# Optimization experiments

Hardware: AMD Instinct MI355X
Metric: run time of the kernel (lower is better)

The kernel has to match this reference:

```python
import jax, jax.numpy as jnp
from jax import lax
import numpy as np

K = 3          # kernel size
KK = K * K
PAD = 1
STRIDE = 1
DIL = 1


def _bilinear_gather(img, ys, xs):
    # img: [B,C,H,W]; ys/xs: [B,KK,Ho,Wo] float sample coords.
    # torchvision deform_conv2d bilinear: zero outside, corner-wise validity.
    B, C, H, W = img.shape
    y0f = jnp.floor(ys)
    x0f = jnp.floor(xs)
    ly = ys - y0f
    lx = xs - x0f
    y0 = y0f.astype(jnp.int32)
    x0 = x0f.astype(jnp.int32)

    def corner(yi, xi):
        valid = (yi >= 0) & (yi < H) & (xi >= 0) & (xi < W)
        yc = jnp.clip(yi, 0, H - 1)
        xc = jnp.clip(xi, 0, W - 1)
        g = jax.vmap(lambda im, y, x: im[:, y, x])(img, yc, xc)  # [B,C,KK,Ho,Wo]
        return g * valid[:, None].astype(img.dtype)

    w00 = ((1 - ly) * (1 - lx))[:, None]
    w01 = ((1 - ly) * lx)[:, None]
    w10 = (ly * (1 - lx))[:, None]
    w11 = (ly * lx)[:, None]
    out = corner(y0, x0) * w00
    out = out + corner(y0, x0 + 1) * w01
    out = out + corner(y0 + 1, x0) * w10
    out = out + corner(y0 + 1, x0 + 1) * w11
    return out  # [B,C,KK,Ho,Wo]


def _deform_conv_forward(x, weight, bias, pg_w, pg_b):
    B, C, H, W = x.shape
    O = weight.shape[0]
    # offset/mask generator: 3x3 conv, stride 1, pad 1 -> [B, 3*KK, H, W]
    params = lax.conv_general_dilated(
        x, pg_w, window_strides=(1, 1), padding=[(1, 1), (1, 1)],
        dimension_numbers=('NCHW', 'OIHW', 'NCHW'))
    params = params + pg_b[None, :, None, None]
    oh, ow, m = jnp.split(params, 3, axis=1)          # each [B,KK,H,W]
    offset = jnp.concatenate([oh, ow], axis=1)        # [B,2*KK,H,W] (as in module)
    mask = jax.nn.sigmoid(m)                          # [B,KK,H,W]

    Ho = (H + 2 * PAD - DIL * (K - 1) - 1) // STRIDE + 1
    Wo = (W + 2 * PAD - DIL * (K - 1) - 1) // STRIDE + 1

    # torchvision layout: channel 2n = dy, 2n+1 = dx for kernel slot n
    off = offset.reshape(B, KK, 2, Ho, Wo)
    dy = off[:, :, 0]  # [B,KK,Ho,Wo]
    dx = off[:, :, 1]

    n = jnp.arange(KK)
    ki = (n // K).astype(x.dtype)   # kernel row offset
    kj = (n % K).astype(x.dtype)    # kernel col offset
    oy = (jnp.arange(Ho, dtype=x.dtype) * STRIDE - PAD)
    ox = (jnp.arange(Wo, dtype=x.dtype) * STRIDE - PAD)
    ys = oy[None, None, :, None] + (DIL * ki)[None, :, None, None] + dy
    xs = ox[None, None, None, :] + (DIL * kj)[None, :, None, None] + dx

    sampled = _bilinear_gather(x, ys, xs)             # [B,C,KK,Ho,Wo]
    sampled = sampled * mask[:, None]                 # modulated (DCNv2)

    w = weight.reshape(O, C, KK)
    out = jnp.einsum('bckhw,ock->bohw', sampled, w)
    out = out + bias[None, :, None, None]
    return out


def setup_inputs() -> dict:
    key = jax.random.key(0)
    k1, k2, k3, k4 = jax.random.split(key, 4)
    B, C, H, W, O = 4, 64, 128, 128, 64
    x = jax.random.normal(k1, (B, C, H, W), dtype=jnp.float32)
    weight = jax.random.normal(k2, (O, C, K, K), dtype=jnp.float32) * 0.05
    bias = jax.random.normal(k3, (O,), dtype=jnp.float32) * 0.05
    pg_w = jax.random.normal(k4, (3 * KK, C, 3, 3), dtype=jnp.float32) * 0.01
    pg_b = jnp.zeros((3 * KK,), dtype=jnp.float32)
    return {'x': x, 'weight': weight, 'bias': bias, 'pg_w': pg_w, 'pg_b': pg_b}


def reference(x, weight, bias, pg_w, pg_b):
    return _deform_conv_forward(x, weight, bias, pg_w, pg_b)
```

## Files before the change

### kernel.cpp

```cpp
#include <hip/hip_runtime.h>
#include <hip/hip_fp16.h>
#include <math.h>


typedef __attribute__((ext_vector_type(8))) short short8;
typedef __attribute__((ext_vector_type(8))) _Float16 f16x8;
typedef __attribute__((ext_vector_type(4))) float f32x4;

#define PSTR 2088

__device__ __forceinline__ unsigned short f2h(float f) {
    union { __half h; unsigned short s; } v; v.h = __float2half_rn(f); return v.s;
}
__device__ __forceinline__ f16x8 s2f(short8 s) {
    union { short8 s; f16x8 f; } u; u.s = s; return u.f;
}
__device__ __forceinline__ __half2 u2h2(unsigned u) {
    union { unsigned u; __half2 h; } v; v.u = u; return v.h;
}
__device__ __forceinline__ unsigned h22u(__half2 h) {
    union { __half2 h; unsigned u; } v; v.h = h; return v.u;
}
__device__ __forceinline__ unsigned uget(const uint4& v, int p) {
    return p == 0 ? v.x : p == 1 ? v.y : p == 2 ? v.z : v.w;
}

__global__ __launch_bounds__(256) void k_prep(const float* __restrict__ x,
                                              unsigned short* __restrict__ xh,
                                              const float* __restrict__ weight,
                                              const float* __restrict__ pg_w,
                                              unsigned short* __restrict__ wtF,
                                              unsigned short* __restrict__ pgwF) {
    __shared__ float tile[64][33];
    int bid = blockIdx.x;
    int t = threadIdx.x;
    if (bid < 2048) {
        int b = bid >> 9, h = (bid >> 2) & 127, w0 = (bid & 3) * 32;
        for (int idx = t; idx < 2048; idx += 256) {
            int c = idx >> 5, w = idx & 31;
            tile[c][w] = x[((b * 64 + c) * 128 + h) * 128 + w0 + w];
        }
        __syncthreads();
        {
            int wl = t >> 3, c0 = (t & 7) * 8;
            short8 v;
#pragma unroll
            for (int e = 0; e < 8; ++e) v[e] = (short)f2h(tile[c0 + e][wl]);
            *(short8*)&xh[(((size_t)b * 128 + h) * 128 + w0 + wl) * 64 + c0] = v;
        }
    } else {
        int idx = (bid - 2048) * 256 + t;
        if (idx < 36864) {
            int e = idx & 7, l = (idx >> 3) & 63, grp = idx >> 9;
            int nt = grp & 3, kb = (grp >> 2) & 1, kk = grp >> 3;
            int ln = l & 15, quad = l >> 4;
            int o = nt * 16 + ln;
            int c = kb * 32 + quad * 8 + e;
            wtF[idx] = f2h(weight[(o * 64 + c) * 9 + kk]);
        }
        int i2 = idx - 36864;
        if (i2 >= 0 && i2 < 18432) {
            int e = i2 & 7, l = (i2 >> 3) & 63, grp = i2 >> 9;
            int tl = grp & 1, kb = grp >> 1;
            int ln = l & 15, quad = l >> 4;
            int p = tl * 16 + ln;
            int k = kb * 32 + quad * 8 + e;
            float v = 0.f;
            if (p < 27) {
                int q = k >> 6, c = k & 63;
                v = pg_w[(p * 64 + c) * 9 + q];
            }
            pgwF[i2] = f2h(v);
        }
    }
}

__global__ __launch_bounds__(512, 4) void k_fused(const unsigned short* __restrict__ xh,
                                                  const unsigned short* __restrict__ pgwF,
                                                  const float* __restrict__ pg_b,
                                                  const unsigned short* __restrict__ wtF,
                                                  const float* __restrict__ bias,
                                                  float* __restrict__ out) {
    __shared__ unsigned short patch[8 * PSTR];
    __shared__ float P_s[27 * 129];

    int bid = blockIdx.x;
    int b  = bid >> 7;
    int h0 = ((bid >> 3) & 15) * 8;
    int w0 = (bid & 7) * 16;
    int t = threadIdx.x;
    int base_y = h0 - 2, base_x = w0 - 2;
    const unsigned short* xbb = xh + (size_t)b * 16384 * 64;

    for (int i = t; i < 2080; i += 512) {
        int yy = i / 160;
        int r  = i - yy * 160;
        int xx = r >> 3;
        int cg = r & 7;
        int gy = base_y + yy, gx = base_x + xx;
        int pos = yy * 20 + xx;
        short8 v = (short8)0;
        if (((unsigned)gy < 128u) && ((unsigned)gx < 128u))
            v = *(const short8*)&xbb[(gy * 128 + gx) * 64 + cg * 8];
        *(short8*)&patch[cg * PSTR + pos * 8] = v;
    }
    __syncthreads();

    int l = t & 63, w = t >> 6;
    int quad = l >> 4, ln = l & 15;
    int px = w * 16 + ln;
    int hh = h0 + w, ww = w0 + ln;

    {
        f32x4 o0 = {0.f, 0.f, 0.f, 0.f}, o1 = {0.f, 0.f, 0.f, 0.f};
#pragma unroll
        for (int kb = 0; kb < 18; ++kb) {
            int q = kb >> 1;
            int kh = q / 3, kw = q - 3 * (q / 3);
            short8 b0 = *(const short8*)&pgwF[(kb * 2 + 0) * 512 + l * 8];
            short8 b1 = *(const short8*)&pgwF[(kb * 2 + 1) * 512 + l * 8];
            int aoff = (w + kh + 1) * 20 + (ln + kw + 1);
            int cg = (kb & 1) * 4 + quad;
            short8 af = *(const short8*)&patch[cg * PSTR + aoff * 8];
            o0 = __builtin_amdgcn_mfma_f32_16x16x32_f16(s2f(af), s2f(b0), o0, 0, 0, 0);
            o1 = __builtin_amdgcn_mfma_f32_16x16x32_f16(s2f(af), s2f(b1), o1, 0, 0, 0);
        }
#pragma unroll
        for (int tile = 0; tile < 2; ++tile) {
            int p = tile * 16 + ln;
            f32x4 a = tile ? o1 : o0;
            if (p < 27) {
                float bo = pg_b[p];
#pragma unroll
                for (int i = 0; i < 4; ++i) {
                    int wpx = w * 16 + quad * 4 + i;
                    float v = a[i] + bo;
                    if (p >= 18) v = 1.f / (1.f + expf(-v));
                    P_s[p * 129 + wpx] = v;
                }
            }
        }
    }
    __syncthreads();

    f32x4 acc[4];
#pragma unroll
    for (int nt = 0; nt < 4; ++nt) acc[nt] = (f32x4){0.f, 0.f, 0.f, 0.f};

    int qbase = quad * PSTR;

#pragma unroll
    for (int kk = 0; kk < 9; ++kk) {
        short8 bfr[2][4];
#pragma unroll
        for (int kb = 0; kb < 2; ++kb)
#pragma unroll
            for (int nt = 0; nt < 4; ++nt)
                bfr[kb][nt] = *(const short8*)&wtF[((kk * 2 + kb) * 4 + nt) * 512 + l * 8];

        int ki = kk / 3, kj = kk - 3 * (kk / 3);
        float dyv = P_s[(2 * kk) * 129 + px];
        float dxv = P_s[(2 * kk + 1) * 129 + px];
        float m   = P_s[(18 + kk) * 129 + px];
        float ys = (float)(hh - 1 + ki) + dyv;
        float xs = (float)(ww - 1 + kj) + dxv;
        float y0f = floorf(ys), x0f = floorf(xs);
        int y0 = (int)y0f, x0 = (int)x0f;
        float ly = ys - y0f, lx = xs - x0f;
        float v0y = ((unsigned)y0 < 128u) ? 1.f : 0.f;
        float v1y = ((unsigned)(y0 + 1) < 128u) ? 1.f : 0.f;
        float v0x = ((unsigned)x0 < 128u) ? 1.f : 0.f;
        float v1x = ((unsigned)(x0 + 1) < 128u) ? 1.f : 0.f;
        float w00 = (1.f - ly) * (1.f - lx) * v0y * v0x * m;
        float w01 = (1.f - ly) * lx * v0y * v1x * m;
        float w10 = ly * (1.f - lx) * v1y * v0x * m;
        float w11 = ly * lx * v1y * v1x * m;
        int ly0 = y0 - base_y, lx0 = x0 - base_x;
        bool inp = ((unsigned)ly0 < 12u) && ((unsigned)lx0 < 18u);

        uint4 r[2][4];
        if (inp) {
            int pb = qbase + (ly0 * 20 + lx0) * 8;
#pragma unroll
            for (int kb = 0; kb < 2; ++kb) {
                int base = pb + kb * 4 * PSTR;
                r[kb][0] = *(const uint4*)&patch[base];
                r[kb][1] = *(const uint4*)&patch[base + 8];
                r[kb][2] = *(const uint4*)&patch[base + 160];
                r[kb][3] = *(const uint4*)&patch[base + 168];
            }
        } else {
            int y0c = min(max(y0, 0), 127), y1c = min(max(y0 + 1, 0), 127);
            int x0c = min(max(x0, 0), 127), x1c = min(max(x0 + 1, 0), 127);
            int base00 = (y0c * 128 + x0c) * 64;
            int dxo = (x1c - x0c) * 64, dyo = (y1c - y0c) * 8192;
#pragma unroll
            for (int kb = 0; kb < 2; ++kb) {
                int c0 = kb * 32 + quad * 8;
                r[kb][0] = *(const uint4*)&xbb[base00 + c0];
                r[kb][1] = *(const uint4*)&xbb[base00 + dxo + c0];
                r[kb][2] = *(const uint4*)&xbb[base00 + dyo + c0];
                r[kb][3] = *(const uint4*)&xbb[base00 + dyo + dxo + c0];
            }
        }

        __half2 W00 = __float2half2_rn(w00), W01 = __float2half2_rn(w01);
        __half2 W10 = __float2half2_rn(w10), W11 = __float2half2_rn(w11);
        f16x8 af[2];
#pragma unroll
        for (int kb = 0; kb < 2; ++kb) {
            union { unsigned u[4]; f16x8 f; } afu;
#pragma unroll
            for (int p = 0; p < 4; ++p) {
                __half2 v = __hmul2(W00, u2h2(uget(r[kb][0], p)));
                v = __hfma2(W01, u2h2(uget(r[kb][1], p)), v);
                v = __hfma2(W10, u2h2(uget(r[kb][2], p)), v);
                v = __hfma2(W11, u2h2(uget(r[kb][3], p)), v);
                afu.u[p] = h22u(v);
            }
            af[kb] = afu.f;
        }

#pragma unroll
        for (int kb = 0; kb < 2; ++kb)
#pragma unroll
            for (int nt = 0; nt < 4; ++nt)
                acc[nt] = __builtin_amdgcn_mfma_f32_16x16x32_f16(af[kb], s2f(bfr[kb][nt]), acc[nt], 0, 0, 0);
    }

    int ehh = h0 + w, eww = w0 + quad * 4;
#pragma unroll
    for (int nt = 0; nt < 4; ++nt) {
        int o = nt * 16 + ln;
        float bo = bias[o];
        float4 v;
        v.x = acc[nt][0] + bo; v.y = acc[nt][1] + bo;
        v.z = acc[nt][2] + bo; v.w = acc[nt][3] + bo;
        *(float4*)&out[((size_t)b * 64 + o) * 16384 + ehh * 128 + eww] = v;
    }
}

extern "C" void kernel_launch(void* const* d_in, const int* in_sizes, int n_in,
                              void* d_out, int out_size, void* d_ws, size_t ws_size,
                              hipStream_t stream) {
    const float* x      = (const float*)d_in[0];
    const float* weight = (const float*)d_in[1];
    const float* bias   = (const float*)d_in[2];
    const float* pg_w   = (const float*)d_in[3];
    const float* pg_b   = (const float*)d_in[4];
    float* out = (float*)d_out;

    unsigned short* xhB  = (unsigned short*)d_ws;
    unsigned short* wtF  = xhB + (size_t)4 * 16384 * 64;
    unsigned short* pgwF = wtF + 36864;

    k_prep<<<2264, 256, 0, stream>>>(x, xhB, weight, pg_w, wtF, pgwF);
    k_fused<<<512, 512, 0, stream>>>(xhB, pgwF, pg_b, wtF, bias, out);
}
```

Before: 98.93 us.

## Drop NHWC fp16 pre-pass; load and convert fp32 NCHW input directly into LDS patch

Removes the separate transpose/convert pass that wrote an NHWC fp16 copy of x to workspace. The fused kernel now reads fp32 NCHW directly when filling its LDS patch, converting pairs of channels to fp16 in place. Out-of-patch bilinear samples gather 32 scalar fp32 loads per corner set instead of vector fp16 loads. It also drops the unroll on the kk loop and the occupancy hint in launch bounds. This saves a full-tensor round trip through global memory and a launch, but makes the patch fill and the fallback gathers uncoalesced and more load-heavy.

```diff
diff --git a/kernel.cpp b/kernel.cpp
--- a/kernel.cpp
+++ b/kernel.cpp
@@ -25,62 +25,41 @@
     return p == 0 ? v.x : p == 1 ? v.y : p == 2 ? v.z : v.w;
 }
 
-__global__ __launch_bounds__(256) void k_prep(const float* __restrict__ x,
-                                              unsigned short* __restrict__ xh,
-                                              const float* __restrict__ weight,
+__global__ __launch_bounds__(256) void k_pack(const float* __restrict__ weight,
                                               const float* __restrict__ pg_w,
                                               unsigned short* __restrict__ wtF,
                                               unsigned short* __restrict__ pgwF) {
-    __shared__ float tile[64][33];
-    int bid = blockIdx.x;
-    int t = threadIdx.x;
-    if (bid < 2048) {
-        int b = bid >> 9, h = (bid >> 2) & 127, w0 = (bid & 3) * 32;
-        for (int idx = t; idx < 2048; idx += 256) {
-            int c = idx >> 5, w = idx & 31;
-            tile[c][w] = x[((b * 64 + c) * 128 + h) * 128 + w0 + w];
-        }
-        __syncthreads();
-        {
-            int wl = t >> 3, c0 = (t & 7) * 8;
-            short8 v;
-#pragma unroll
-            for (int e = 0; e < 8; ++e) v[e] = (short)f2h(tile[c0 + e][wl]);
-            *(short8*)&xh[(((size_t)b * 128 + h) * 128 + w0 + wl) * 64 + c0] = v;
-        }
-    } else {
-        int idx = (bid - 2048) * 256 + t;
-        if (idx < 36864) {
-            int e = idx & 7, l = (idx >> 3) & 63, grp = idx >> 9;
-            int nt = grp & 3, kb = (grp >> 2) & 1, kk = grp >> 3;
-            int ln = l & 15, quad = l >> 4;
-            int o = nt * 16 + ln;
-            int c = kb * 32 + quad * 8 + e;
-            wtF[idx] = f2h(weight[(o * 64 + c) * 9 + kk]);
-        }
-        int i2 = idx - 36864;
-        if (i2 >= 0 && i2 < 18432) {
-            int e = i2 & 7, l = (i2 >> 3) & 63, grp = i2 >> 9;
-            int tl = grp & 1, kb = grp >> 1;
-            int ln = l & 15, quad = l >> 4;
-            int p = tl * 16 + ln;
-            int k = kb * 32 + quad * 8 + e;
-            float v = 0.f;
-            if (p < 27) {
-                int q = k >> 6, c = k & 63;
-                v = pg_w[(p * 64 + c) * 9 + q];
-            }
-            pgwF[i2] = f2h(v);
-        }
-    }
-}
-
-__global__ __launch_bounds__(512, 4) void k_fused(const unsigned short* __restrict__ xh,
-                                                  const unsigned short* __restrict__ pgwF,
-                                                  const float* __restrict__ pg_b,
-                                                  const unsigned short* __restrict__ wtF,
-                                                  const float* __restrict__ bias,
-                                                  float* __restrict__ out) {
+    int idx = blockIdx.x * 256 + threadIdx.x;
+    if (idx < 36864) {
+        int e = idx & 7, l = (idx >> 3) & 63, grp = idx >> 9;
+        int nt = grp & 3, kb = (grp >> 2) & 1, kk = grp >> 3;
+        int ln = l & 15, quad = l >> 4;
+        int o = nt * 16 + ln;
+        int c = kb * 32 + quad * 8 + e;
+        wtF[idx] = f2h(weight[(o * 64 + c) * 9 + kk]);
+    }
+    int i2 = idx - 36864;
+    if (i2 >= 0 && i2 < 18432) {
+        int e = i2 & 7, l = (i2 >> 3) & 63, grp = i2 >> 9;
+        int tl = grp & 1, kb = grp >> 1;
+        int ln = l & 15, quad = l >> 4;
+        int p = tl * 16 + ln;
+        int k = kb * 32 + quad * 8 + e;
+        float v = 0.f;
+        if (p < 27) {
+            int q = k >> 6, c = k & 63;
+            v = pg_w[(p * 64 + c) * 9 + q];
+        }
+        pgwF[i2] = f2h(v);
+    }
+}
+
+__global__ __launch_bounds__(512) void k_fused(const float* __restrict__ x,
+                                               const unsigned short* __restrict__ pgwF,
+                                               const float* __restrict__ pg_b,
+                                               const unsigned short* __restrict__ wtF,
+                                               const float* __restrict__ bias,
+                                               float* __restrict__ out) {
     __shared__ unsigned short patch[8 * PSTR];
     __shared__ float P_s[27 * 129];
 
@@ -90,19 +69,23 @@
     int w0 = (bid & 7) * 16;
     int t = threadIdx.x;
     int base_y = h0 - 2, base_x = w0 - 2;
-    const unsigned short* xbb = xh + (size_t)b * 16384 * 64;
-
-    for (int i = t; i < 2080; i += 512) {
-        int yy = i / 160;
-        int r  = i - yy * 160;
-        int xx = r >> 3;
-        int cg = r & 7;
+    const float* xb0 = x + (size_t)b * 64 * 16384;
+
+    for (int i = t; i < 8320; i += 512) {
+        int cp  = i / 260;
+        int rem = i - cp * 260;
+        int yy  = rem / 20;
+        int xx  = rem - yy * 20;
         int gy = base_y + yy, gx = base_x + xx;
+        unsigned u = 0;
+        if (((unsigned)gy < 128u) && ((unsigned)gx < 128u)) {
+            int c = cp * 2;
+            float f0 = xb0[(c * 128 + gy) * 128 + gx];
+            float f1 = xb0[((c + 1) * 128 + gy) * 128 + gx];
+            u = (unsigned)f2h(f0) | ((unsigned)f2h(f1) << 16);
+        }
         int pos = yy * 20 + xx;
-        short8 v = (short8)0;
-        if (((unsigned)gy < 128u) && ((unsigned)gx < 128u))
-            v = *(const short8*)&xbb[(gy * 128 + gx) * 64 + cg * 8];
-        *(short8*)&patch[cg * PSTR + pos * 8] = v;
+        *(unsigned*)&patch[(cp >> 2) * PSTR + pos * 8 + (cp & 3) * 2] = u;
     }
     __syncthreads();
 
@@ -149,7 +132,6 @@
 
     int qbase = quad * PSTR;
 
-#pragma unroll
     for (int kk = 0; kk < 9; ++kk) {
         short8 bfr[2][4];
 #pragma unroll
@@ -192,15 +174,22 @@
         } else {
             int y0c = min(max(y0, 0), 127), y1c = min(max(y0 + 1, 0), 127);
             int x0c = min(max(x0, 0), 127), x1c = min(max(x0 + 1, 0), 127);
-            int base00 = (y0c * 128 + x0c) * 64;
-            int dxo = (x1c - x0c) * 64, dyo = (y1c - y0c) * 8192;
+            int yc[4] = {y0c, y0c, y1c, y1c};
+            int xc[4] = {x0c, x1c, x0c, x1c};
 #pragma unroll
             for (int kb = 0; kb < 2; ++kb) {
                 int c0 = kb * 32 + quad * 8;
-                r[kb][0] = *(const uint4*)&xbb[base00 + c0];
-                r[kb][1] = *(const uint4*)&xbb[base00 + dxo + c0];
-                r[kb][2] = *(const uint4*)&xbb[base00 + dyo + c0];
-                r[kb][3] = *(const uint4*)&xbb[base00 + dyo + dxo + c0];
+#pragma unroll
+                for (int cr = 0; cr < 4; ++cr) {
+                    union { unsigned u[4]; uint4 v; } tmp;
+#pragma unroll
+                    for (int e = 0; e < 4; ++e) {
+                        float f0 = xb0[((c0 + 2 * e) * 128 + yc[cr]) * 128 + xc[cr]];
+                        float f1 = xb0[((c0 + 2 * e + 1) * 128 + yc[cr]) * 128 + xc[cr]];
+                        tmp.u[e] = (unsigned)f2h(f0) | ((unsigned)f2h(f1) << 16);
+                    }
+                    r[kb][cr] = tmp.v;
+                }
             }
         }
 
@@ -250,10 +239,9 @@
     const float* pg_b   = (const float*)d_in[4];
     float* out = (float*)d_out;
 
-    unsigned short* xhB  = (unsigned short*)d_ws;
-    unsigned short* wtF  = xhB + (size_t)4 * 16384 * 64;
+    unsigned short* wtF  = (unsigned short*)d_ws;
     unsigned short* pgwF = wtF + 36864;
 
-    k_prep<<<2264, 256, 0, stream>>>(x, xhB, weight, pg_w, wtF, pgwF);
-    k_fused<<<512, 512, 0, stream>>>(xhB, pgwF, pg_b, wtF, bias, out);
-}
+    k_pack<<<216, 256, 0, stream>>>(weight, pg_w, wtF, pgwF);
+    k_fused<<<512, 512, 0, stream>>>(x, pgwF, pg_b, wtF, bias, out);
+}
```

Result: slower. 115.6 us (+16.9%).

## Software-pipeline bilinear gather reads across kernel taps with wave-uniform fallback

Applied to the files above, without the earlier changes.

Restructures the 9-tap sampling loop into a software pipeline. The shared-memory corner reads for the next tap and channel half are issued before the current half's conversion and MFMA. Patch reads now always run from a clamped address, and the global-memory fallback is taken only when some lane falls outside the patch, checked through a wave-wide any. Loading weights per half and keeping the loop rolled lowers register pressure, but the loop-carried state and loads that are sometimes overwritten add instructions.

```diff
diff --git a/kernel.cpp b/kernel.cpp
--- a/kernel.cpp
+++ b/kernel.cpp
@@ -17,9 +17,6 @@
 }
 __device__ __forceinline__ __half2 u2h2(unsigned u) {
     union { unsigned u; __half2 h; } v; v.u = u; return v.h;
-}
-__device__ __forceinline__ unsigned h22u(__half2 h) {
-    union { __half2 h; unsigned u; } v; v.h = h; return v.u;
 }
 __device__ __forceinline__ unsigned uget(const uint4& v, int p) {
     return p == 0 ? v.x : p == 1 ? v.y : p == 2 ? v.z : v.w;
@@ -75,6 +72,70 @@
     }
 }
 
+#define PARAMS(KK, W00_, W01_, W10_, W11_, PB_, INP_, Y0_, X0_)                   \
+    {                                                                             \
+        int ki_ = (KK) / 3, kj_ = (KK) - 3 * ((KK) / 3);                          \
+        float dyv_ = P_s[(2 * (KK)) * 129 + px];                                  \
+        float dxv_ = P_s[(2 * (KK) + 1) * 129 + px];                              \
+        float mm_  = P_s[(18 + (KK)) * 129 + px];                                 \
+        float ys_ = (float)(hh - 1 + ki_) + dyv_;                                 \
+        float xs_ = (float)(ww - 1 + kj_) + dxv_;                                 \
+        float y0f_ = floorf(ys_), x0f_ = floorf(xs_);                             \
+        int y0_ = (int)y0f_, x0_ = (int)x0f_;                                     \
+        float ly_ = ys_ - y0f_, lx_ = xs_ - x0f_;                                 \
+        float v0y_ = ((unsigned)y0_ < 128u) ? 1.f : 0.f;                          \
+        float v1y_ = ((unsigned)(y0_ + 1) < 128u) ? 1.f : 0.f;                    \
+        float v0x_ = ((unsigned)x0_ < 128u) ? 1.f : 0.f;                          \
+        float v1x_ = ((unsigned)(x0_ + 1) < 128u) ? 1.f : 0.f;                    \
+        W00_ = __float2half2_rn((1.f - ly_) * (1.f - lx_) * v0y_ * v0x_ * mm_);   \
+        W01_ = __float2half2_rn((1.f - ly_) * lx_ * v0y_ * v1x_ * mm_);           \
+        W10_ = __float2half2_rn(ly_ * (1.f - lx_) * v1y_ * v0x_ * mm_);           \
+        W11_ = __float2half2_rn(ly_ * lx_ * v1y_ * v1x_ * mm_);                   \
+        int ly0_ = y0_ - base_y, lx0_ = x0_ - base_x;                             \
+        INP_ = ((unsigned)ly0_ < 12u) && ((unsigned)lx0_ < 18u);                  \
+        int ly0c_ = min(max(ly0_, 0), 11), lx0c_ = min(max(lx0_, 0), 17);         \
+        PB_ = qbase + (ly0c_ * 20 + lx0c_) * 8;                                   \
+        Y0_ = y0_; X0_ = x0_;                                                     \
+    }
+
+#define RD4(DST, BASE)                                                            \
+    { DST[0] = *(const uint4*)&patch[(BASE)];                                     \
+      DST[1] = *(const uint4*)&patch[(BASE) + 8];                                 \
+      DST[2] = *(const uint4*)&patch[(BASE) + 160];                               \
+      DST[3] = *(const uint4*)&patch[(BASE) + 168]; }
+
+#define FIX(DST, KB, INP, Y0, X0)                                                 \
+    if (__any(!(INP))) { if (!(INP)) {                                            \
+        int y0c_ = min(max((Y0), 0), 127), y1c_ = min(max((Y0) + 1, 0), 127);     \
+        int x0c_ = min(max((X0), 0), 127), x1c_ = min(max((X0) + 1, 0), 127);     \
+        int b00_ = (y0c_ * 128 + x0c_) * 64;                                      \
+        int dxo_ = (x1c_ - x0c_) * 64, dyo_ = (y1c_ - y0c_) * 8192;               \
+        int c0_ = (KB) * 32 + quad * 8;                                           \
+        DST[0] = *(const uint4*)&xbb[b00_ + c0_];                                 \
+        DST[1] = *(const uint4*)&xbb[b00_ + dxo_ + c0_];                          \
+        DST[2] = *(const uint4*)&xbb[b00_ + dyo_ + c0_];                          \
+        DST[3] = *(const uint4*)&xbb[b00_ + dyo_ + dxo_ + c0_]; } }
+
+#define CVTMMA(RSET, KK, KB, W00_, W01_, W10_, W11_)                              \
+    {                                                                             \
+        short8 bfr_[4];                                                           \
+        _Pragma("unroll")                                                         \
+        for (int nt = 0; nt < 4; ++nt)                                            \
+            bfr_[nt] = *(const short8*)&wtF[(((KK) * 2 + (KB)) * 4 + nt) * 512 + l * 8]; \
+        union { unsigned u[4]; f16x8 f; } afu_;                                   \
+        _Pragma("unroll")                                                         \
+        for (int p = 0; p < 4; ++p) {                                             \
+            __half2 v_ = __hmul2(W00_, u2h2(uget(RSET[0], p)));                   \
+            v_ = __hfma2(W01_, u2h2(uget(RSET[1], p)), v_);                       \
+            v_ = __hfma2(W10_, u2h2(uget(RSET[2], p)), v_);                       \
+            v_ = __hfma2(W11_, u2h2(uget(RSET[3], p)), v_);                       \
+            afu_.u[p] = *(unsigned*)&v_;                                          \
+        }                                                                         \
+        _Pragma("unroll")                                                         \
+        for (int nt = 0; nt < 4; ++nt)                                            \
+            acc[nt] = __builtin_amdgcn_mfma_f32_16x16x32_f16(afu_.f, s2f(bfr_[nt]), acc[nt], 0, 0, 0); \
+    }
+
 __global__ __launch_bounds__(512, 4) void k_fused(const unsigned short* __restrict__ xh,
                                                   const unsigned short* __restrict__ pgwF,
                                                   const float* __restrict__ pg_b,
@@ -149,83 +210,26 @@
 
     int qbase = quad * PSTR;
 
-#pragma unroll
+    __half2 W00, W01, W10, W11, nW00, nW01, nW10, nW11;
+    int pb, npb, y0c, x0c, ny0, nx0;
+    bool inp, ninp;
+    uint4 rA[4], rB[4];
+
+    PARAMS(0, W00, W01, W10, W11, pb, inp, y0c, x0c);
+    RD4(rA, pb);
+
     for (int kk = 0; kk < 9; ++kk) {
-        short8 bfr[2][4];
-#pragma unroll
-        for (int kb = 0; kb < 2; ++kb)
-#pragma unroll
-            for (int nt = 0; nt < 4; ++nt)
-                bfr[kb][nt] = *(const short8*)&wtF[((kk * 2 + kb) * 4 + nt) * 512 + l * 8];
-
-        int ki = kk / 3, kj = kk - 3 * (kk / 3);
-        float dyv = P_s[(2 * kk) * 129 + px];
-        float dxv = P_s[(2 * kk + 1) * 129 + px];
-        float m   = P_s[(18 + kk) * 129 + px];
-        float ys = (float)(hh - 1 + ki) + dyv;
-        float xs = (float)(ww - 1 + kj) + dxv;
-        float y0f = floorf(ys), x0f = floorf(xs);
-        int y0 = (int)y0f, x0 = (int)x0f;
-        float ly = ys - y0f, lx = xs - x0f;
-        float v0y = ((unsigned)y0 < 128u) ? 1.f : 0.f;
-        float v1y = ((unsigned)(y0 + 1) < 128u) ? 1.f : 0.f;
-        float v0x = ((unsigned)x0 < 128u) ? 1.f : 0.f;
-        float v1x = ((unsigned)(x0 + 1) < 128u) ? 1.f : 0.f;
-        float w00 = (1.f - ly) * (1.f - lx) * v0y * v0x * m;
-        float w01 = (1.f - ly) * lx * v0y * v1x * m;
-        float w10 = ly * (1.f - lx) * v1y * v0x * m;
-        float w11 = ly * lx * v1y * v1x * m;
-        int ly0 = y0 - base_y, lx0 = x0 - base_x;
-        bool inp = ((unsigned)ly0 < 12u) && ((unsigned)lx0 < 18u);
-
-        uint4 r[2][4];
-        if (inp) {
-            int pb = qbase + (ly0 * 20 + lx0) * 8;
-#pragma unroll
-            for (int kb = 0; kb < 2; ++kb) {
-                int base = pb + kb * 4 * PSTR;
-                r[kb][0] = *(const uint4*)&patch[base];
-                r[kb][1] = *(const uint4*)&patch[base + 8];
-                r[kb][2] = *(const uint4*)&patch[base + 160];
-                r[kb][3] = *(const uint4*)&patch[base + 168];
-            }
-        } else {
-            int y0c = min(max(y0, 0), 127), y1c = min(max(y0 + 1, 0), 127);
-            int x0c = min(max(x0, 0), 127), x1c = min(max(x0 + 1, 0), 127);
-            int base00 = (y0c * 128 + x0c) * 64;
-            int dxo = (x1c - x0c) * 64, dyo = (y1c - y0c) * 8192;
-#pragma unroll
-            for (int kb = 0; kb < 2; ++kb) {
-                int c0 = kb * 32 + quad * 8;
-                r[kb][0] = *(const uint4*)&xbb[base00 + c0];
-                r[kb][1] = *(const uint4*)&xbb[base00 + dxo + c0];
-                r[kb][2] = *(const uint4*)&xbb[base00 + dyo + c0];
-                r[kb][3] = *(const uint4*)&xbb[base00 + dyo + dxo + c0];
-            }
-        }
-
-        __half2 W00 = __float2half2_rn(w00), W01 = __float2half2_rn(w01);
-        __half2 W10 = __float2half2_rn(w10), W11 = __float2half2_rn(w11);
-        f16x8 af[2];
-#pragma unroll
-        for (int kb = 0; kb < 2; ++kb) {
-            union { unsigned u[4]; f16x8 f; } afu;
-#pragma unroll
-            for (int p = 0; p < 4; ++p) {
-                __half2 v = __hmul2(W00, u2h2(uget(r[kb][0], p)));
-                v = __hfma2(W01, u2h2(uget(r[kb][1], p)), v);
-                v = __hfma2(W10, u2h2(uget(r[kb][2], p)), v);
-                v = __hfma2(W11, u2h2(uget(r[kb][3], p)), v);
-                afu.u[p] = h22u(v);
-            }
-            af[kb] = afu.f;
-        }
-
-#pragma unroll
-        for (int kb = 0; kb < 2; ++kb)
-#pragma unroll
-            for (int nt = 0; nt < 4; ++nt)
-                acc[nt] = __builtin_amdgcn_mfma_f32_16x16x32_f16(af[kb], s2f(bfr[kb][nt]), acc[nt], 0, 0, 0);
+        RD4(rB, pb + 4 * PSTR);
+        FIX(rA, 0, inp, y0c, x0c);
+        CVTMMA(rA, kk, 0, W00, W01, W10, W11);
+        if (kk < 8) {
+            PARAMS(kk + 1, nW00, nW01, nW10, nW11, npb, ninp, ny0, nx0);
+            RD4(rA, npb);
+        }
+        FIX(rB, 1, inp, y0c, x0c);
+        CVTMMA(rB, kk, 1, W00, W01, W10, W11);
+        W00 = nW00; W01 = nW01; W10 = nW10; W11 = nW11;
+        pb = npb; inp = ninp; y0c = ny0; x0c = nx0;
     }
 
     int ehh = h0 + w, eww = w0 + quad * 4;
```

Result: no change. 97.53 us (-1.4%).
